# Kernel tuning notes

Measured on AMD Instinct MI355X. Metric: run time of the kernel, lower is better.

Reference implementation:

```python
import jax, jax.numpy as jnp
import numpy as np

B, S, H = 32, 4096, 1024  # batch, seq_len, hidden_size; enc feature dim = 2*H


def setup_inputs() -> dict:
    key = jax.random.key(0)
    k1, k2, k3, k4 = jax.random.split(key, 4)
    hidden = jax.random.normal(k1, (B, H), dtype=jnp.float32)
    encoder_outputs = jax.random.normal(k2, (B, S, 2 * H), dtype=jnp.float32)
    # nn.Linear(2H, H) params, scaled like torch default init
    W = jax.random.normal(k3, (H, 2 * H), dtype=jnp.float32) * (1.0 / np.sqrt(2 * H))
    b = jax.random.normal(k4, (H,), dtype=jnp.float32) * (1.0 / np.sqrt(2 * H))
    return {"hidden": hidden, "encoder_outputs": encoder_outputs, "W": W, "b": b}


def reference(hidden, encoder_outputs, W, b):
    # tmp = Linear(encoder_outputs): [B,S,H]
    tmp = jnp.einsum("bsd,hd->bsh", encoder_outputs, W) + b
    # energies[b,s] = hidden[b] . tmp[b,s]  (the original's double Python loop)
    energies = jnp.einsum("bh,bsh->bs", hidden, tmp)
    # F.softmax over dim=1 (the seq dim for a 2D tensor), then unsqueeze(1)
    attn = jax.nn.softmax(energies, axis=-1)
    return attn[:, None, :]  # [B, 1, S]
```

## Files before the change

kernel.cpp:

```cpp
#include <hip/hip_runtime.h>
#include <math.h>

#define BB 32
#define SS 4096
#define HH 1024
#define TWOH 2048

__global__ __launch_bounds__(256) void proj_kernel(
    const float* __restrict__ hidden,
    const float* __restrict__ W,
    float* __restrict__ v)
{
    __shared__ float lh[BB][32];
    const int tid  = threadIdx.x;
    const int dblk = blockIdx.x;
    const int hc   = blockIdx.y;
    const int h0   = hc * 32;

    for (int i = tid; i < BB * 32; i += 256) {
        const int b = i >> 5, hh = i & 31;
        lh[b][hh] = hidden[b * HH + h0 + hh];
    }
    __syncthreads();

    const int d0 = dblk * 512 + tid * 2;
    float2 acc[BB];
#pragma unroll
    for (int b = 0; b < BB; ++b) acc[b] = make_float2(0.f, 0.f);

    for (int hh = 0; hh < 32; ++hh) {
        const float2 w = *reinterpret_cast<const float2*>(&W[(size_t)(h0 + hh) * TWOH + d0]);
#pragma unroll
        for (int b = 0; b < BB; ++b) {
            const float hb = lh[b][hh];
            acc[b].x += hb * w.x;
            acc[b].y += hb * w.y;
        }
    }
#pragma unroll
    for (int b = 0; b < BB; ++b) {
        atomicAdd(&v[b * TWOH + d0],     acc[b].x);
        atomicAdd(&v[b * TWOH + d0 + 1], acc[b].y);
    }
}

__global__ __launch_bounds__(256) void energies_kernel(
    const float* __restrict__ enc,
    const float* __restrict__ v,
    float* __restrict__ energies)
{
    const int tid  = threadIdx.x;
    const int wave = tid >> 6;
    const int lane = tid & 63;
    const int rowBase = blockIdx.x * 64;
    const int b = rowBase >> 12;

    const float4* v4 = reinterpret_cast<const float4*>(v + (size_t)b * TWOH);
    float4 vf[8];
#pragma unroll
    for (int j = 0; j < 8; ++j) vf[j] = v4[j * 64 + lane];

    const int row0 = rowBase + wave * 16;
    for (int r = 0; r < 16; ++r) {
        const int row = row0 + r;
        const float4* e4 = reinterpret_cast<const float4*>(enc + (size_t)row * TWOH);
        float acc = 0.f;
#pragma unroll
        for (int j = 0; j < 8; ++j) {
            const float4 e = e4[j * 64 + lane];
            acc += vf[j].x * e.x + vf[j].y * e.y + vf[j].z * e.z + vf[j].w * e.w;
        }
#pragma unroll
        for (int m = 32; m >= 1; m >>= 1) acc += __shfl_xor(acc, m, 64);
        if (lane == 0) energies[row] = acc;
    }
}

__global__ __launch_bounds__(256) void softmax_kernel(float* __restrict__ out)
{
    const int b   = blockIdx.x;
    const int tid = threadIdx.x;
    float* row = out + (size_t)b * SS;

    float x[16];
#pragma unroll
    for (int k = 0; k < 16; ++k) x[k] = row[tid + k * 256];

    float mx = -INFINITY;
#pragma unroll
    for (int k = 0; k < 16; ++k) mx = fmaxf(mx, x[k]);

    __shared__ float red[8];
    const int wave = tid >> 6, lane = tid & 63;
#pragma unroll
    for (int m = 32; m >= 1; m >>= 1) mx = fmaxf(mx, __shfl_xor(mx, m, 64));
    if (lane == 0) red[wave] = mx;
    __syncthreads();
    mx = fmaxf(fmaxf(red[0], red[1]), fmaxf(red[2], red[3]));

    float sum = 0.f;
#pragma unroll
    for (int k = 0; k < 16; ++k) { x[k] = __expf(x[k] - mx); sum += x[k]; }
#pragma unroll
    for (int m = 32; m >= 1; m >>= 1) sum += __shfl_xor(sum, m, 64);
    if (lane == 0) red[4 + wave] = sum;
    __syncthreads();
    sum = red[4] + red[5] + red[6] + red[7];

    const float inv = 1.f / sum;
#pragma unroll
    for (int k = 0; k < 16; ++k) row[tid + k * 256] = x[k] * inv;
}

extern "C" void kernel_launch(void* const* d_in, const int* in_sizes, int n_in,
                              void* d_out, int out_size, void* d_ws, size_t ws_size,
                              hipStream_t stream)
{
    const float* hidden = (const float*)d_in[0];
    const float* enc    = (const float*)d_in[1];
    const float* W      = (const float*)d_in[2];

    float* v   = (float*)d_ws;
    float* out = (float*)d_out;

    hipMemsetAsync(d_ws, 0, (size_t)BB * TWOH * sizeof(float), stream);

    proj_kernel<<<dim3(4, 32), 256, 0, stream>>>(hidden, W, v);
    energies_kernel<<<dim3(BB * SS / 64), 256, 0, stream>>>(enc, v, out);
    softmax_kernel<<<dim3(BB), 256, 0, stream>>>(out);
}
```

Measured before the change: 1.406 ms.

## Replace atomic projection accumulation with partial buffers plus reduce; prefetch encoder rows

```diff
diff --git a/kernel.cpp b/kernel.cpp
--- a/kernel.cpp
+++ b/kernel.cpp
@@ -5,20 +5,22 @@
 #define SS 4096
 #define HH 1024
 #define TWOH 2048
+#define PPARTS 16
+#define HCHUNK 64
 
 __global__ __launch_bounds__(256) void proj_kernel(
     const float* __restrict__ hidden,
     const float* __restrict__ W,
-    float* __restrict__ v)
+    float* __restrict__ v_part)
 {
-    __shared__ float lh[BB][32];
+    __shared__ float lh[BB][HCHUNK];
     const int tid  = threadIdx.x;
     const int dblk = blockIdx.x;
     const int hc   = blockIdx.y;
-    const int h0   = hc * 32;
+    const int h0   = hc * HCHUNK;
 
-    for (int i = tid; i < BB * 32; i += 256) {
-        const int b = i >> 5, hh = i & 31;
+    for (int i = tid; i < BB * HCHUNK; i += 256) {
+        const int b = i >> 6, hh = i & 63;
         lh[b][hh] = hidden[b * HH + h0 + hh];
     }
     __syncthreads();
@@ -28,8 +30,9 @@
 #pragma unroll
     for (int b = 0; b < BB; ++b) acc[b] = make_float2(0.f, 0.f);
 
-    for (int hh = 0; hh < 32; ++hh) {
-        const float2 w = *reinterpret_cast<const float2*>(&W[(size_t)(h0 + hh) * TWOH + d0]);
+    for (int hh = 0; hh < HCHUNK; ++hh) {
+        const float2 w = *reinterpret_cast<const float2*>(
+            &W[(size_t)(h0 + hh) * TWOH + d0]);
 #pragma unroll
         for (int b = 0; b < BB; ++b) {
             const float hb = lh[b][hh];
@@ -37,11 +40,25 @@
             acc[b].y += hb * w.y;
         }
     }
+
+    float* dst = v_part + (size_t)hc * BB * TWOH;
 #pragma unroll
-    for (int b = 0; b < BB; ++b) {
-        atomicAdd(&v[b * TWOH + d0],     acc[b].x);
-        atomicAdd(&v[b * TWOH + d0 + 1], acc[b].y);
+    for (int b = 0; b < BB; ++b)
+        *reinterpret_cast<float2*>(&dst[b * TWOH + d0]) = acc[b];
+}
+
+__global__ __launch_bounds__(256) void reduce_kernel(
+    const float* __restrict__ v_part,
+    float* __restrict__ v)
+{
+    const int i = (blockIdx.x * 256 + threadIdx.x) * 4;
+    float4 s = make_float4(0.f, 0.f, 0.f, 0.f);
+#pragma unroll
+    for (int p = 0; p < PPARTS; ++p) {
+        const float4 t = *reinterpret_cast<const float4*>(&v_part[(size_t)p * BB * TWOH + i]);
+        s.x += t.x; s.y += t.y; s.z += t.z; s.w += t.w;
     }
+    *reinterpret_cast<float4*>(&v[i]) = s;
 }
 
 __global__ __launch_bounds__(256) void energies_kernel(
@@ -61,18 +78,36 @@
     for (int j = 0; j < 8; ++j) vf[j] = v4[j * 64 + lane];
 
     const int row0 = rowBase + wave * 16;
+
+    float4 cur[8];
+    {
+        const float4* e4 = reinterpret_cast<const float4*>(enc + (size_t)row0 * TWOH);
+#pragma unroll
+        for (int j = 0; j < 8; ++j) cur[j] = e4[j * 64 + lane];
+    }
+
     for (int r = 0; r < 16; ++r) {
-        const int row = row0 + r;
-        const float4* e4 = reinterpret_cast<const float4*>(enc + (size_t)row * TWOH);
+        float4 nxt[8];
+        if (r < 15) {
+            const float4* n4 = reinterpret_cast<const float4*>(
+                enc + (size_t)(row0 + r + 1) * TWOH);
+#pragma unroll
+            for (int j = 0; j < 8; ++j) nxt[j] = n4[j * 64 + lane];
+        }
+
         float acc = 0.f;
 #pragma unroll
-        for (int j = 0; j < 8; ++j) {
-            const float4 e = e4[j * 64 + lane];
-            acc += vf[j].x * e.x + vf[j].y * e.y + vf[j].z * e.z + vf[j].w * e.w;
-        }
+        for (int j = 0; j < 8; ++j)
+            acc += vf[j].x * cur[j].x + vf[j].y * cur[j].y
+                 + vf[j].z * cur[j].z + vf[j].w * cur[j].w;
 #pragma unroll
         for (int m = 32; m >= 1; m >>= 1) acc += __shfl_xor(acc, m, 64);
-        if (lane == 0) energies[row] = acc;
+        if (lane == 0) energies[row0 + r] = acc;
+
+        if (r < 15) {
+#pragma unroll
+            for (int j = 0; j < 8; ++j) cur[j] = nxt[j];
+        }
     }
 }
 
@@ -120,12 +155,12 @@
     const float* enc    = (const float*)d_in[1];
     const float* W      = (const float*)d_in[2];
 
-    float* v   = (float*)d_ws;
-    float* out = (float*)d_out;
+    float* v_part = (float*)d_ws;
+    float* v      = v_part + (size_t)PPARTS * BB * TWOH;
+    float* out    = (float*)d_out;
 
-    hipMemsetAsync(d_ws, 0, (size_t)BB * TWOH * sizeof(float), stream);
-
-    proj_kernel<<<dim3(4, 32), 256, 0, stream>>>(hidden, W, v);
+    proj_kernel   <<<dim3(4, PPARTS), 256, 0, stream>>>(hidden, W, v_part);
+    reduce_kernel <<<dim3(64),        256, 0, stream>>>(v_part, v);
     energies_kernel<<<dim3(BB * SS / 64), 256, 0, stream>>>(enc, v, out);
-    softmax_kernel<<<dim3(BB), 256, 0, stream>>>(out);
+    softmax_kernel<<<dim3(BB),        256, 0, stream>>>(out);
 }
```

New measurement: 1.365 ms. 1.03x faster.
